# Kernel optimization log

Hardware: AMD Instinct MI355X
Metric: run time of the kernel (lower is better)

## Reference

```python
import jax, jax.numpy as jnp
import numpy as np
from functools import partial

ENC = 128  # encoding_dim

def setup_inputs() -> dict:
    key = jax.random.key(0)
    ks = jax.random.split(key, 6)
    B, S, E, H = 8, 512, 128, 512
    action_sequence = jax.random.normal(ks[0], (B, S, E), dtype=jnp.float32)
    # nn.Linear-style init scale ~ 1/sqrt(fan_in)
    W1 = jax.random.normal(ks[1], (H, E), dtype=jnp.float32) / np.sqrt(E)
    b1 = jnp.zeros((H,), dtype=jnp.float32)
    W2 = jax.random.normal(ks[2], (ENC * ENC, H), dtype=jnp.float32) / np.sqrt(H)
    b2 = jnp.zeros((ENC * ENC,), dtype=jnp.float32)
    e0 = jax.random.normal(ks[3], (1, ENC), dtype=jnp.float32) / 10.0
    return {"action_sequence": action_sequence, "W1": W1, "b1": b1,
            "W2": W2, "b2": b2, "e0": e0}

def reference(action_sequence, W1, b1, W2, b2, e0):
    B, S, E = action_sequence.shape
    # fast-weight generation: two dense layers
    hidden = jnp.tanh(jnp.einsum('bse,he->bsh', action_sequence, W1) + b1)
    Wa = (jnp.einsum('bsh,oh->bso', hidden, W2) + b2).reshape(B, S, ENC, ENC)
    # attractor dynamics: et_{i} = clamp(et_{i-1} @ Wa[:, i], -5, 5)
    e0b = jnp.broadcast_to(e0, (B, ENC))
    Wa_seq = jnp.transpose(Wa[:, 1:], (1, 0, 2, 3))  # [S-1, B, ENC, ENC]
    def step(et, Wa_i):
        et_next = jnp.clip(jnp.einsum('bd,bde->be', et, Wa_i), -5.0, 5.0)
        return et_next, et_next
    _, es = jax.lax.scan(step, e0b, Wa_seq)  # [S-1, B, ENC]
    encodings = jnp.concatenate([e0b[None], es], axis=0)  # [S, B, ENC]
    return jnp.transpose(encodings, (1, 0, 2))  # [B, S, ENC]
```

## Files before the change

### kernel.cpp

```cpp
#include <hip/hip_runtime.h>
#include <cstddef>

#define BB 8
#define SS 512
#define EE 128
#define HH 512
#define ENC 128

__device__ __forceinline__ float xla_tanhf(float x) {
    const float cx = fminf(fmaxf(x, -9.0f), 9.0f);
    const float x2 = __fmul_rn(cx, cx);
    float p = -2.76076847742355e-16f;
    p = __fadd_rn(__fmul_rn(p, x2), 2.00018790482477e-13f);
    p = __fadd_rn(__fmul_rn(p, x2), -8.60467152213735e-11f);
    p = __fadd_rn(__fmul_rn(p, x2), 5.12229709037114e-08f);
    p = __fadd_rn(__fmul_rn(p, x2), 1.48572235717979e-05f);
    p = __fadd_rn(__fmul_rn(p, x2), 6.37261928875436e-04f);
    p = __fadd_rn(__fmul_rn(p, x2), 4.89352455891786e-03f);
    const float num = __fmul_rn(cx, p);
    float q = 1.19825839466702e-06f;
    q = __fadd_rn(__fmul_rn(q, x2), 1.18534705686654e-04f);
    q = __fadd_rn(__fmul_rn(q, x2), 2.26843463243900e-03f);
    q = __fadd_rn(__fmul_rn(q, x2), 4.89352518554385e-03f);
    const float r = __fdiv_rn(num, q);
    return (fabsf(x) < 0.0004f) ? x : r;
}

__device__ __forceinline__ int arow_map(int m, int chm1, int chsh, int i0) {
    return ((m >> chsh) * SS) + i0 + (m & chm1);
}

template <int ACT, int MAPROW, int TRANSP>
__device__ __forceinline__ void gemm_body(const float* __restrict__ A,
                                          const float* __restrict__ Bm,
                                          const float* __restrict__ bias,
                                          float* __restrict__ C,
                                          int N, int K,
                                          int chm1, int chsh, int i0,
                                          int bx, int by,
                                          float (*As)[128], float (*Bs)[128]) {
    const int tid = threadIdx.x;
    const int tx = tid & 15;
    const int ty = tid >> 4;
    const int n0 = bx * 128;
    const int m0 = by * 128;
    const int bd = bx >> 4;
    const int be = bx & 15;

    const int lr = tid >> 2;
    const int lc = (tid & 3) << 2;

    const int ga0 = MAPROW ? arow_map(m0 + lr, chm1, chsh, i0) : (m0 + lr);
    const int ga1 = MAPROW ? arow_map(m0 + lr + 64, chm1, chsh, i0) : (m0 + lr + 64);

    const int r0 = lr, r1 = lr + 64;
    const int gb0 = TRANSP ? ((bd * 16 + (r0 >> 3)) * 128 + be * 8 + (r0 & 7))
                           : (n0 + r0);
    const int gb1 = TRANSP ? ((bd * 16 + (r1 >> 3)) * 128 + be * 8 + (r1 & 7))
                           : (n0 + r1);

    float acc[8][8];
#pragma unroll
    for (int i = 0; i < 8; ++i)
#pragma unroll
        for (int j = 0; j < 8; ++j) acc[i][j] = 0.f;

    for (int k0 = 0; k0 < K; k0 += 16) {
        const float4 a0 = *(const float4*)(A + (size_t)ga0 * K + (k0 + lc));
        const float4 a1 = *(const float4*)(A + (size_t)ga1 * K + (k0 + lc));
        const float4 b0 = *(const float4*)(Bm + (size_t)gb0 * K + (k0 + lc));
        const float4 b1 = *(const float4*)(Bm + (size_t)gb1 * K + (k0 + lc));

        __syncthreads();

        As[lc + 0][lr] = a0.x; As[lc + 1][lr] = a0.y;
        As[lc + 2][lr] = a0.z; As[lc + 3][lr] = a0.w;
        As[lc + 0][lr + 64] = a1.x; As[lc + 1][lr + 64] = a1.y;
        As[lc + 2][lr + 64] = a1.z; As[lc + 3][lr + 64] = a1.w;
        Bs[lc + 0][lr] = b0.x; Bs[lc + 1][lr] = b0.y;
        Bs[lc + 2][lr] = b0.z; Bs[lc + 3][lr] = b0.w;
        Bs[lc + 0][lr + 64] = b1.x; Bs[lc + 1][lr + 64] = b1.y;
        Bs[lc + 2][lr + 64] = b1.z; Bs[lc + 3][lr + 64] = b1.w;

        __syncthreads();

#pragma unroll
        for (int k = 0; k < 16; ++k) {
            const float4 av0 = *(const float4*)&As[k][ty * 8];
            const float4 av1 = *(const float4*)&As[k][ty * 8 + 4];
            const float4 bv0 = *(const float4*)&Bs[k][tx * 8];
            const float4 bv1 = *(const float4*)&Bs[k][tx * 8 + 4];
            const float a[8] = {av0.x, av0.y, av0.z, av0.w, av1.x, av1.y, av1.z, av1.w};
            const float b[8] = {bv0.x, bv0.y, bv0.z, bv0.w, bv1.x, bv1.y, bv1.z, bv1.w};
#pragma unroll
            for (int i = 0; i < 8; ++i)
#pragma unroll
                for (int j = 0; j < 8; ++j)
                    acc[i][j] = __fadd_rn(acc[i][j], __fmul_rn(a[i], b[j]));
        }
    }

#pragma unroll
    for (int i = 0; i < 8; ++i) {
        const int m = m0 + ty * 8 + i;
        if (TRANSP) {
            const int d = bd * 16 + tx;
#pragma unroll
            for (int j = 0; j < 8; ++j) {
                const int ee = be * 8 + j;
                const int o = d * 128 + ee;
                const float v = __fadd_rn(acc[i][j], bias[o]);
                C[(size_t)m * N + ((size_t)(d >> 2) * 128 + ee) * 4 + (d & 3)] = v;
            }
        } else {
            float v[8];
#pragma unroll
            for (int j = 0; j < 8; ++j) {
                const int n = n0 + tx * 8 + j;
                v[j] = __fadd_rn(acc[i][j], bias[n]);
                if (ACT) v[j] = xla_tanhf(v[j]);
            }
            float4* dst = (float4*)(C + (size_t)m * N + (n0 + tx * 8));
            dst[0] = make_float4(v[0], v[1], v[2], v[3]);
            dst[1] = make_float4(v[4], v[5], v[6], v[7]);
        }
    }
}

template <int ACT, int MAPROW, int TRANSP>
__global__ __launch_bounds__(256) void gemm_nt(const float* __restrict__ A,
                                               const float* __restrict__ Bm,
                                               const float* __restrict__ bias,
                                               float* __restrict__ C,
                                               int N, int K,
                                               int chm1, int chsh, int i0) {
    __shared__ float As[16][128];
    __shared__ float Bs[16][128];
    gemm_body<ACT, MAPROW, TRANSP>(A, Bm, bias, C, N, K, chm1, chsh, i0,
                                   blockIdx.x, blockIdx.y, As, Bs);
}

#define SCAN_QUARTER(Q, WC, WP)                                             \
    {                                                                       \
                                                             \
        const int pf = (ii - start) * 4 + (Q) + 3;                          \
        const int pfc = (pf < nq) ? pf : (nq - 1);      \
        const float4* P4 = Wb4 + (size_t)(start + (pfc >> 2)) * 4096        \
                               + (size_t)(pfc & 3) * 1024 + e;              \
        _Pragma("unroll")                                                   \
        for (int u = 0; u < 8; ++u) WP[u] = P4[u * 128];                    \
        asm volatile("" ::: "memory");                                      \
              \
        _Pragma("unroll")                                                   \
        for (int dq = 0; dq < 8; ++dq) {                                    \
            const float4 t4 = *(const float4*)&et[s][(Q) * 32 + dq * 4];    \
            const float4 wv = WC[dq];        \
            sum = __fadd_rn(sum, __fmul_rn(t4.x, wv.x));                    \
            sum = __fadd_rn(sum, __fmul_rn(t4.y, wv.y));                    \
            sum = __fadd_rn(sum, __fmul_rn(t4.z, wv.z));                    \
            sum = __fadd_rn(sum, __fmul_rn(t4.w, wv.w));                    \
        }                                                                   \
    }

__device__ __forceinline__ void scan_body(const float* __restrict__ Wa,
                                          const float* __restrict__ e0,
                                          float* __restrict__ et_state,
                                          float* __restrict__ out,
                                          int i0, int CH, int b,
                                          float (*et)[128]) {
    const int e = threadIdx.x & 127;

    int s = 0;
    if (i0 == 0) {
        const float v = e0[e];
        et[0][e] = v;
        out[(size_t)b * SS * ENC + e] = v;
    } else {
        et[0][e] = et_state[b * 128 + e];
    }
    __syncthreads();

    const int start = (i0 == 0) ? 1 : 0;
    const float4* Wb4 = (const float4*)(Wa + (size_t)b * CH * (ENC * ENC));
    const int nq = (CH - start) * 4;

    float4 w0[8], w1[8], w2[8], w3[8];

    {
        const float4* S4 = Wb4 + (size_t)start * 4096 + e;
#pragma unroll
        for (int u = 0; u < 8; ++u) w0[u] = S4[u * 128];
#pragma unroll
        for (int u = 0; u < 8; ++u) w1[u] = S4[(8 + u) * 128];
#pragma unroll
        for (int u = 0; u < 8; ++u) w2[u] = S4[(16 + u) * 128];
    }
    asm volatile("" ::: "memory");

    for (int ii = start; ii < CH; ++ii) {
        float sum = 0.f;
        SCAN_QUARTER(0, w0, w3)
        SCAN_QUARTER(1, w1, w0)
        SCAN_QUARTER(2, w2, w1)
        SCAN_QUARTER(3, w3, w2)
        const float v = fminf(fmaxf(sum, -5.f), 5.f);
        out[((size_t)b * SS + (i0 + ii)) * ENC + e] = v;
        et[s ^ 1][e] = v;
        __syncthreads();
        s ^= 1;
    }
    et_state[b * 128 + e] = et[s][e];
}

__global__ __launch_bounds__(128, 1) void scan_kernel(const float* __restrict__ Wa,
                                                      const float* __restrict__ e0,
                                                      float* __restrict__ et_state,
                                                      float* __restrict__ out,
                                                      int i0, int CH) {
    __shared__ float et[2][128];
    scan_body(Wa, e0, et_state, out, i0, CH, blockIdx.x, et);
}

__global__ __launch_bounds__(256, 1) void gemm2_scan(
        const float* __restrict__ hidden, const float* __restrict__ W2,
        const float* __restrict__ b2, float* __restrict__ WaDst,
        const float* __restrict__ WaSrc, const float* __restrict__ e0,
        float* __restrict__ et_state, float* __restrict__ out,
        int chm1, int chsh, int i0_g2, int i0_scan, int CH) {
    __shared__ float As[16][128];
    __shared__ float Bs[16][128];
    __shared__ float et[2][128];

    if (blockIdx.x < 8) {
        if (blockIdx.y != 0) return;
        __builtin_amdgcn_s_setprio(2);
        scan_body(WaSrc, e0, et_state, out, i0_scan, CH, blockIdx.x, et);
        return;
    }
    gemm_body<0, 1, 1>(hidden, W2, b2, WaDst, ENC * ENC, HH,
                       chm1, chsh, i0_g2, blockIdx.x - 8, blockIdx.y, As, Bs);
}

extern "C" void kernel_launch(void* const* d_in, const int* in_sizes, int n_in,
                              void* d_out, int out_size, void* d_ws, size_t ws_size,
                              hipStream_t stream) {
    const float* A  = (const float*)d_in[0];
    const float* W1 = (const float*)d_in[1];
    const float* b1 = (const float*)d_in[2];
    const float* W2 = (const float*)d_in[3];
    const float* b2 = (const float*)d_in[4];
    const float* e0 = (const float*)d_in[5];
    float* out = (float*)d_out;

    const size_t hid_bytes = (size_t)BB * SS * HH * sizeof(float);

    int CH = 0;
    for (int c = 64; c >= 16; c >>= 1) {
        const size_t chunk_bytes = (size_t)BB * c * (size_t)(ENC * ENC) * sizeof(float);
        if (4096 + hid_bytes + 2 * chunk_bytes <= ws_size) { CH = c; break; }
    }

    if (CH != 0) {
        const int Mc = BB * CH;
        int chsh = 0;
        while ((1 << chsh) < CH) ++chsh;
        const int chm1 = CH - 1;
        const int n = SS / CH;

        float* et_state = (float*)d_ws;
        float* hidden   = (float*)((char*)d_ws + 4096);
        float* Wa0 = hidden + (size_t)BB * SS * HH;
        float* Wa1 = Wa0 + (size_t)Mc * (ENC * ENC);
        float* Wab[2] = {Wa0, Wa1};

        dim3 g1(HH / 128, (BB * SS) / 128);
        gemm_nt<1, 0, 0><<<g1, 256, 0, stream>>>(A, W1, b1, hidden, HH, EE,
                                                 0, 0, 0);
        dim3 g2((ENC * ENC) / 128, Mc / 128);
        gemm_nt<0, 1, 1><<<g2, 256, 0, stream>>>(hidden, W2, b2, Wa0,
                                                 ENC * ENC, HH, chm1, chsh, 0);
        for (int c = 0; c < n; ++c) {
            if (c + 1 < n) {
                dim3 gc(8 + (ENC * ENC) / 128, Mc / 128);
                gemm2_scan<<<gc, 256, 0, stream>>>(hidden, W2, b2,
                                                   Wab[(c + 1) & 1], Wab[c & 1],
                                                   e0, et_state, out,
                                                   chm1, chsh,
                                                   (c + 1) * CH, c * CH, CH);
            } else {
                scan_kernel<<<BB, 128, 0, stream>>>(Wab[c & 1], e0, et_state,
                                                    out, c * CH, CH);
            }
        }
        return;
    }

    int CHs = 16;
    for (int c = 512; c >= 16; c >>= 1) {
        const size_t Mc = (size_t)BB * c;
        const size_t need = 4096 + Mc * HH * sizeof(float) +
                            Mc * (size_t)(ENC * ENC) * sizeof(float);
        if (need <= ws_size) { CHs = c; break; }
    }
    const int Mc = BB * CHs;
    int chsh = 0;
    while ((1 << chsh) < CHs) ++chsh;
    const int chm1 = CHs - 1;

    float* et_state = (float*)d_ws;
    float* hidden   = (float*)((char*)d_ws + 4096);
    float* Wa       = hidden + (size_t)Mc * HH;

    for (int i0 = 0; i0 < SS; i0 += CHs) {
        dim3 g1(HH / 128, Mc / 128);
        gemm_nt<1, 1, 0><<<g1, 256, 0, stream>>>(A, W1, b1, hidden, HH, EE,
                                                 chm1, chsh, i0);
        dim3 g2((ENC * ENC) / 128, Mc / 128);
        gemm_nt<0, 0, 1><<<g2, 256, 0, stream>>>(hidden, W2, b2, Wa, ENC * ENC,
                                                 HH, 0, 0, 0);
        scan_kernel<<<BB, 128, 0, stream>>>(Wa, e0, et_state, out, i0, CHs);
    }
}
```

Baseline: 1.673 ms.

## Restructure chunked GEMM/scan pipeline with larger chunks and simpler scan prefetch

Fixes the chunk size at 128 steps and computes the hidden layer per chunk instead of all at once, so the hidden buffer only holds one chunk. The Wa chunk buffers get padding between them, the combined GEMM2+scan kernel uses a plain row mapping and allows more blocks per CU, and the idle upper half of the 256-thread scan blocks exits early. Inside the scan, prefetching now loads the next step's matching quarter after each quarter is consumed, through a running pointer, with all four register buffers preloaded. This aims to cut launch count and address arithmetic and keep the scan's loads streaming. The cost is an extra GEMM1 launch per chunk and a prefetch pointer that reads past the end of the chunk on the last step, into the padding.

```diff
diff --git a/kernel.cpp b/kernel.cpp
--- a/kernel.cpp
+++ b/kernel.cpp
@@ -140,26 +140,23 @@
                                    blockIdx.x, blockIdx.y, As, Bs);
 }
 
-#define SCAN_QUARTER(Q, WC, WP)                                             \
+#define SCAN_Q4(Q, BUF)                                                     \
     {                                                                       \
-                                                             \
-        const int pf = (ii - start) * 4 + (Q) + 3;                          \
-        const int pfc = (pf < nq) ? pf : (nq - 1);      \
-        const float4* P4 = Wb4 + (size_t)(start + (pfc >> 2)) * 4096        \
-                               + (size_t)(pfc & 3) * 1024 + e;              \
-        _Pragma("unroll")                                                   \
-        for (int u = 0; u < 8; ++u) WP[u] = P4[u * 128];                    \
-        asm volatile("" ::: "memory");                                      \
               \
         _Pragma("unroll")                                                   \
         for (int dq = 0; dq < 8; ++dq) {                                    \
             const float4 t4 = *(const float4*)&et[s][(Q) * 32 + dq * 4];    \
-            const float4 wv = WC[dq];        \
+            const float4 wv = BUF[dq];       \
             sum = __fadd_rn(sum, __fmul_rn(t4.x, wv.x));                    \
             sum = __fadd_rn(sum, __fmul_rn(t4.y, wv.y));                    \
             sum = __fadd_rn(sum, __fmul_rn(t4.z, wv.z));                    \
             sum = __fadd_rn(sum, __fmul_rn(t4.w, wv.w));                    \
         }                                                                   \
+         \
+        _Pragma("unroll")                                                   \
+        for (int u = 0; u < 8; ++u) BUF[u] = Pf[u * 128];                   \
+        Pf += 1024;                                                         \
+        asm volatile("" ::: "memory");                                      \
     }
 
 __device__ __forceinline__ void scan_body(const float* __restrict__ Wa,
@@ -182,27 +179,26 @@
 
     const int start = (i0 == 0) ? 1 : 0;
     const float4* Wb4 = (const float4*)(Wa + (size_t)b * CH * (ENC * ENC));
-    const int nq = (CH - start) * 4;
 
     float4 w0[8], w1[8], w2[8], w3[8];
-
-    {
-        const float4* S4 = Wb4 + (size_t)start * 4096 + e;
-#pragma unroll
-        for (int u = 0; u < 8; ++u) w0[u] = S4[u * 128];
-#pragma unroll
-        for (int u = 0; u < 8; ++u) w1[u] = S4[(8 + u) * 128];
-#pragma unroll
-        for (int u = 0; u < 8; ++u) w2[u] = S4[(16 + u) * 128];
-    }
+    const float4* Pq = Wb4 + (size_t)start * 4096 + e;
+#pragma unroll
+    for (int u = 0; u < 8; ++u) w0[u] = Pq[u * 128];
+#pragma unroll
+    for (int u = 0; u < 8; ++u) w1[u] = Pq[(8 + u) * 128];
+#pragma unroll
+    for (int u = 0; u < 8; ++u) w2[u] = Pq[(16 + u) * 128];
+#pragma unroll
+    for (int u = 0; u < 8; ++u) w3[u] = Pq[(24 + u) * 128];
+    const float4* Pf = Pq + 4096;
     asm volatile("" ::: "memory");
 
     for (int ii = start; ii < CH; ++ii) {
         float sum = 0.f;
-        SCAN_QUARTER(0, w0, w3)
-        SCAN_QUARTER(1, w1, w0)
-        SCAN_QUARTER(2, w2, w1)
-        SCAN_QUARTER(3, w3, w2)
+        SCAN_Q4(0, w0)
+        SCAN_Q4(1, w1)
+        SCAN_Q4(2, w2)
+        SCAN_Q4(3, w3)
         const float v = fminf(fmaxf(sum, -5.f), 5.f);
         out[((size_t)b * SS + (i0 + ii)) * ENC + e] = v;
         et[s ^ 1][e] = v;
@@ -221,24 +217,25 @@
     scan_body(Wa, e0, et_state, out, i0, CH, blockIdx.x, et);
 }
 
-__global__ __launch_bounds__(256, 1) void gemm2_scan(
+__global__ __launch_bounds__(256, 3) void gemm2_scan(
         const float* __restrict__ hidden, const float* __restrict__ W2,
         const float* __restrict__ b2, float* __restrict__ WaDst,
         const float* __restrict__ WaSrc, const float* __restrict__ e0,
         float* __restrict__ et_state, float* __restrict__ out,
-        int chm1, int chsh, int i0_g2, int i0_scan, int CH) {
+        int i0_scan, int CH) {
     __shared__ float As[16][128];
     __shared__ float Bs[16][128];
     __shared__ float et[2][128];
 
     if (blockIdx.x < 8) {
         if (blockIdx.y != 0) return;
+        if (threadIdx.x >= 128) return;
         __builtin_amdgcn_s_setprio(2);
         scan_body(WaSrc, e0, et_state, out, i0_scan, CH, blockIdx.x, et);
         return;
     }
-    gemm_body<0, 1, 1>(hidden, W2, b2, WaDst, ENC * ENC, HH,
-                       chm1, chsh, i0_g2, blockIdx.x - 8, blockIdx.y, As, Bs);
+    gemm_body<0, 0, 1>(hidden, W2, b2, WaDst, ENC * ENC, HH,
+                       0, 0, 0, blockIdx.x - 8, blockIdx.y, As, Bs);
 }
 
 extern "C" void kernel_launch(void* const* d_in, const int* in_sizes, int n_in,
@@ -252,41 +249,42 @@
     const float* e0 = (const float*)d_in[5];
     float* out = (float*)d_out;
 
-    const size_t hid_bytes = (size_t)BB * SS * HH * sizeof(float);
-
-    int CH = 0;
-    for (int c = 64; c >= 16; c >>= 1) {
-        const size_t chunk_bytes = (size_t)BB * c * (size_t)(ENC * ENC) * sizeof(float);
-        if (4096 + hid_bytes + 2 * chunk_bytes <= ws_size) { CH = c; break; }
-    }
-
-    if (CH != 0) {
-        const int Mc = BB * CH;
-        int chsh = 0;
-        while ((1 << chsh) < CH) ++chsh;
-        const int chm1 = CH - 1;
-        const int n = SS / CH;
-
+    const int CH = 128;
+    const int n = SS / CH;
+    const int Mc = BB * CH;
+    const size_t hid_bytes = (size_t)Mc * HH * sizeof(float);
+    const size_t chunk_elems = (size_t)Mc * (ENC * ENC);
+    const size_t wa_pad_bytes = chunk_elems * sizeof(float) + 65536;
+    const size_t need = 4096 + hid_bytes + 2 * wa_pad_bytes;
+
+    if (need <= ws_size) {
         float* et_state = (float*)d_ws;
         float* hidden   = (float*)((char*)d_ws + 4096);
-        float* Wa0 = hidden + (size_t)BB * SS * HH;
-        float* Wa1 = Wa0 + (size_t)Mc * (ENC * ENC);
+        float* Wa0 = (float*)((char*)hidden + hid_bytes);
+        float* Wa1 = (float*)((char*)Wa0 + wa_pad_bytes);
         float* Wab[2] = {Wa0, Wa1};
 
-        dim3 g1(HH / 128, (BB * SS) / 128);
-        gemm_nt<1, 0, 0><<<g1, 256, 0, stream>>>(A, W1, b1, hidden, HH, EE,
-                                                 0, 0, 0);
+        const int chm1 = CH - 1;
+        const int chsh = 7;
+
+        dim3 g1(HH / 128, Mc / 128);
         dim3 g2((ENC * ENC) / 128, Mc / 128);
-        gemm_nt<0, 1, 1><<<g2, 256, 0, stream>>>(hidden, W2, b2, Wa0,
-                                                 ENC * ENC, HH, chm1, chsh, 0);
+        dim3 gc(8 + (ENC * ENC) / 128, Mc / 128);
+
+        gemm_nt<1, 1, 0><<<g1, 256, 0, stream>>>(A, W1, b1, hidden, HH, EE,
+                                                 chm1, chsh, 0);
+        gemm_nt<0, 0, 1><<<g2, 256, 0, stream>>>(hidden, W2, b2, Wa0,
+                                                 ENC * ENC, HH, 0, 0, 0);
         for (int c = 0; c < n; ++c) {
             if (c + 1 < n) {
-                dim3 gc(8 + (ENC * ENC) / 128, Mc / 128);
+                gemm_nt<1, 1, 0><<<g1, 256, 0, stream>>>(A, W1, b1, hidden,
+                                                         HH, EE, chm1, chsh,
+                                                         (c + 1) * CH);
                 gemm2_scan<<<gc, 256, 0, stream>>>(hidden, W2, b2,
-                                                   Wab[(c + 1) & 1], Wab[c & 1],
+                                                   Wab[(c + 1) & 1],
+                                                   Wab[c & 1],
                                                    e0, et_state, out,
-                                                   chm1, chsh,
-                                                   (c + 1) * CH, c * CH, CH);
+                                                   c * CH, CH);
             } else {
                 scan_kernel<<<BB, 128, 0, stream>>>(Wab[c & 1], e0, et_state,
                                                     out, c * CH, CH);
@@ -297,25 +295,25 @@
 
     int CHs = 16;
     for (int c = 512; c >= 16; c >>= 1) {
-        const size_t Mc = (size_t)BB * c;
-        const size_t need = 4096 + Mc * HH * sizeof(float) +
-                            Mc * (size_t)(ENC * ENC) * sizeof(float);
-        if (need <= ws_size) { CHs = c; break; }
-    }
-    const int Mc = BB * CHs;
+        const size_t Mcs = (size_t)BB * c;
+        const size_t ned = 4096 + Mcs * HH * sizeof(float) +
+                           Mcs * (size_t)(ENC * ENC) * sizeof(float) + 65536;
+        if (ned <= ws_size) { CHs = c; break; }
+    }
+    const int Mcs = BB * CHs;
     int chsh = 0;
     while ((1 << chsh) < CHs) ++chsh;
     const int chm1 = CHs - 1;
 
     float* et_state = (float*)d_ws;
     float* hidden   = (float*)((char*)d_ws + 4096);
-    float* Wa       = hidden + (size_t)Mc * HH;
+    float* Wa       = hidden + (size_t)Mcs * HH;
 
     for (int i0 = 0; i0 < SS; i0 += CHs) {
-        dim3 g1(HH / 128, Mc / 128);
+        dim3 g1(HH / 128, Mcs / 128);
         gemm_nt<1, 1, 0><<<g1, 256, 0, stream>>>(A, W1, b1, hidden, HH, EE,
                                                  chm1, chsh, i0);
-        dim3 g2((ENC * ENC) / 128, Mc / 128);
+        dim3 g2((ENC * ENC) / 128, Mcs / 128);
         gemm_nt<0, 0, 1><<<g2, 256, 0, stream>>>(hidden, W2, b2, Wa, ENC * ENC,
                                                  HH, 0, 0, 0);
         scan_kernel<<<BB, 128, 0, stream>>>(Wa, e0, et_state, out, i0, CHs);
```

New measurement: 2.040 ms. 22.0% more time.
